# Performance work log

Hardware: AMD Instinct MI355X
Metric: run time of the kernel (lower is better)

## Reference

```python
import jax, jax.numpy as jnp
import numpy as np

INIT_RANGE = 0.02

def setup_inputs() -> dict:
    key = jax.random.key(0)
    ks = jax.random.split(key, 5)
    B, S, D, H, Dh = 4, 2048, 768, 12, 64
    residual = jax.random.normal(ks[0], (B, S, D), dtype=jnp.float32)
    W_Q = jax.random.normal(ks[1], (H, D, Dh), dtype=jnp.float32) * INIT_RANGE
    W_K = jax.random.normal(ks[2], (H, D, Dh), dtype=jnp.float32) * INIT_RANGE
    W_V = jax.random.normal(ks[3], (H, D, Dh), dtype=jnp.float32) * INIT_RANGE
    W_O = jax.random.normal(ks[4], (H, Dh, D), dtype=jnp.float32) * INIT_RANGE
    b_Q = jnp.zeros((H, Dh), dtype=jnp.float32)
    b_K = jnp.zeros((H, Dh), dtype=jnp.float32)
    b_V = jnp.zeros((H, Dh), dtype=jnp.float32)
    b_O = jnp.zeros((D,), dtype=jnp.float32)
    return {"residual": residual, "W_Q": W_Q, "W_K": W_K, "W_V": W_V,
            "W_O": W_O, "b_Q": b_Q, "b_K": b_K, "b_V": b_V, "b_O": b_O}

def reference(residual, W_Q, W_K, W_V, W_O, b_Q, b_K, b_V, b_O):
    # residual: [b, s, d]; W_{Q,K,V}: [h, d, dh]; W_O: [h, dh, d]
    d_head = W_Q.shape[-1]
    q = jnp.einsum('bsd,hde->bshe', residual, W_Q) + b_Q  # [b, s, h, dh]
    k = jnp.einsum('bsd,hde->bshe', residual, W_K) + b_K
    v = jnp.einsum('bsd,hde->bshe', residual, W_V) + b_V
    scores = jnp.einsum('bqhe,bkhe->bhqk', q, k) / jnp.sqrt(jnp.float32(d_head))
    S = residual.shape[1]
    causal = jnp.tril(jnp.ones((S, S), dtype=bool))  # True where attending allowed
    scores = jnp.where(causal, scores, -jnp.inf)
    pattern = jax.nn.softmax(scores, axis=-1)  # [b, h, q, k]
    z = jnp.einsum('bkhe,bhqk->bqhe', v, pattern)  # [b, q, h, dh]
    attn_out = jnp.einsum('bqhe,hed->bqd', z, W_O) + b_O
    return attn_out
```

## Files before the change

### kernel.cpp

```cpp
#include <hip/hip_runtime.h>

typedef short short8 __attribute__((ext_vector_type(8)));
typedef float floatx4 __attribute__((ext_vector_type(4)));
typedef unsigned short ushort_t;


__device__ inline ushort_t f2bf(float f) {
  union { float f; unsigned u; } x; x.f = f;
  unsigned u = x.u;
  unsigned r = u + 0x7fffu + ((u >> 16) & 1u);
  return (ushort_t)(r >> 16);
}

__device__ inline unsigned cvtpk(float a, float b) {
  unsigned r;
  asm("v_cvt_pk_bf16_f32 %0, %1, %2" : "=v"(r) : "v"(a), "v"(b));
  return r;
}

__device__ inline float fexp2(float x) {
#if __has_builtin(__builtin_amdgcn_exp2f)
  return __builtin_amdgcn_exp2f(x);
#else
  return exp2f(x);
#endif
}

__device__ inline void async16(const void* g, void* l) {
  __builtin_amdgcn_global_load_lds((const __attribute__((address_space(1))) void*)g,
                                   (__attribute__((address_space(3))) void*)l,
                                   16, 0, 0);
}


__global__ __launch_bounds__(256) void conv_prep(
    const float* __restrict__ x, ushort_t* __restrict__ rx,
    const float* __restrict__ wq, const float* __restrict__ wk, const float* __restrict__ wv,
    const float* __restrict__ wo,
    const float* __restrict__ bq, const float* __restrict__ bk, const float* __restrict__ bv,
    ushort_t* __restrict__ wqkvT, ushort_t* __restrict__ woT, float* __restrict__ bqkv)
{
  __shared__ ushort_t t[64 * 72];
  const int tid = threadIdx.x;
  const int bid0 = blockIdx.x;
  if (bid0 < 6144) {
    int i = bid0 * 256 + tid;
    float4 f = ((const float4*)x)[i];
    ushort4 o;
    o.x = f2bf(f.x); o.y = f2bf(f.y); o.z = f2bf(f.z); o.w = f2bf(f.w);
    ((ushort4*)rx)[i] = o;
    return;
  }
  const int bid = bid0 - 6144;
  if (bid < 432) {
    int m = bid / 144, rem = bid % 144;
    int h = rem / 12, dt = rem % 12;
    int d0 = dt * 64;
    const float* w = (m == 0) ? wq : ((m == 1) ? wk : wv);
    const float* src = w + ((size_t)h * 768 + d0) * 64;
#pragma unroll
    for (int i = 0; i < 4; ++i) {
      int task = i * 256 + tid;
      int row = task >> 4, c4 = task & 15;
      float4 f = *(const float4*)(src + row * 64 + c4 * 4);
      ushort4 o4;
      o4.x = f2bf(f.x); o4.y = f2bf(f.y); o4.z = f2bf(f.z); o4.w = f2bf(f.w);
      *(ushort4*)&t[row * 72 + c4 * 4] = o4;
    }
    __syncthreads();
    ushort_t* dst = wqkvT + ((size_t)m * 768 + h * 64) * 768 + d0;
#pragma unroll
    for (int i = 0; i < 2; ++i) {
      int task = i * 256 + tid;
      int e = task >> 3, sc = task & 7;
      short8 d8;
#pragma unroll
      for (int j = 0; j < 8; ++j) d8[j] = (short)t[(sc * 8 + j) * 72 + e];
      *(short8*)(dst + (size_t)e * 768 + sc * 8) = d8;
    }
  } else if (bid < 576) {
    int b2 = bid - 432;
    int het = b2 / 12, dt = b2 % 12;
    int he0 = het * 64, d0 = dt * 64;
    const float* src = wo + (size_t)he0 * 768 + d0;
#pragma unroll
    for (int i = 0; i < 4; ++i) {
      int task = i * 256 + tid;
      int row = task >> 4, c4 = task & 15;
      float4 f = *(const float4*)(src + (size_t)row * 768 + c4 * 4);
      ushort4 o4;
      o4.x = f2bf(f.x); o4.y = f2bf(f.y); o4.z = f2bf(f.z); o4.w = f2bf(f.w);
      *(ushort4*)&t[row * 72 + c4 * 4] = o4;
    }
    __syncthreads();
    ushort_t* dst = woT + (size_t)d0 * 768 + he0;
#pragma unroll
    for (int i = 0; i < 2; ++i) {
      int task = i * 256 + tid;
      int dd = task >> 3, sc = task & 7;
      short8 d8;
#pragma unroll
      for (int j = 0; j < 8; ++j) d8[j] = (short)t[(sc * 8 + j) * 72 + dd];
      *(short8*)(dst + (size_t)dd * 768 + sc * 8) = d8;
    }
  } else {
    for (int idx = tid; idx < 2304; idx += 256) {
      int m = idx / 768, rem = idx - m * 768;
      const float* bp = (m == 0) ? bq : ((m == 1) ? bk : bv);
      bqkv[idx] = bp[rem];
    }
  }
}


__global__ __launch_bounds__(256) void gemm_qkv(
    const ushort_t* __restrict__ A, const ushort_t* __restrict__ Bt,
    const float* __restrict__ bias,
    ushort_t* __restrict__ q, ushort_t* __restrict__ k, ushort_t* __restrict__ vt)
{
  __shared__ __align__(16) ushort_t sh[32768];
  const int tid = threadIdx.x;
  const int wave = tid >> 6, lane = tid & 63;
  const int ln15 = lane & 15, quad = lane >> 4;
  const int id = blockIdx.x;
  const int xk = id & 7, j = id >> 3;
  const int bx = (xk >> 1) * 16 + (j & 15);
  const int by = (xk & 1) * 9 + (j >> 4);
  const int row0 = bx * 128, col0 = by * 128;
  const int wm = (wave >> 1) * 64, wn = (wave & 1) * 64;

  const int sr = tid >> 3;
  const int sc = (tid & 7) ^ (sr & 7);
  const ushort_t* gA0 = A + (size_t)(row0 + sr) * 768 + sc * 8;
  const ushort_t* gB0 = Bt + (size_t)(col0 + sr) * 768 + sc * 8;

  const int l7 = ln15 & 7;
  const int baA = (wm + ln15) * 64;
  const int baB = (wn + ln15) * 64;
  const int sl0 = (quad ^ l7) * 8;
  const int sl1 = ((quad + 4) ^ l7) * 8;

  floatx4 acc[4][4];
#pragma unroll
  for (int mi = 0; mi < 4; ++mi)
#pragma unroll
    for (int ni = 0; ni < 4; ++ni)
      acc[mi][ni] = (floatx4){0.f, 0.f, 0.f, 0.f};

#pragma unroll
  for (int i = 0; i < 4; ++i) {
    async16(gA0 + i * 32 * 768, &sh[(i * 256 + tid) * 8]);
    async16(gB0 + i * 32 * 768, &sh[16384 + (i * 256 + tid) * 8]);
  }
  __syncthreads();

  for (int kt = 0; kt < 12; ++kt) {
    const int buf = kt & 1;
    if (kt + 1 < 12) {
      ushort_t* dA = &sh[(buf ^ 1) * 8192];
      ushort_t* dB = &sh[16384 + (buf ^ 1) * 8192];
      const ushort_t* ga = gA0 + (kt + 1) * 64;
      const ushort_t* gb = gB0 + (kt + 1) * 64;
#pragma unroll
      for (int i = 0; i < 4; ++i) {
        async16(ga + i * 32 * 768, dA + (i * 256 + tid) * 8);
        async16(gb + i * 32 * 768, dB + (i * 256 + tid) * 8);
      }
    }
    const ushort_t* sA = &sh[buf * 8192];
    const ushort_t* sB = &sh[16384 + buf * 8192];
    short8 af[4][2], bfv[4][2];
#pragma unroll
    for (int mi = 0; mi < 4; ++mi) {
      af[mi][0] = *(const short8*)&sA[baA + mi * 1024 + sl0];
      af[mi][1] = *(const short8*)&sA[baA + mi * 1024 + sl1];
    }
#pragma unroll
    for (int ni = 0; ni < 4; ++ni) {
      bfv[ni][0] = *(const short8*)&sB[baB + ni * 1024 + sl0];
      bfv[ni][1] = *(const short8*)&sB[baB + ni * 1024 + sl1];
    }
#pragma unroll
    for (int mi = 0; mi < 4; ++mi)
#pragma unroll
      for (int ni = 0; ni < 4; ++ni) {
        acc[mi][ni] = __builtin_amdgcn_mfma_f32_16x16x32_bf16(af[mi][0], bfv[ni][0], acc[mi][ni], 0, 0, 0);
        acc[mi][ni] = __builtin_amdgcn_mfma_f32_16x16x32_bf16(af[mi][1], bfv[ni][1], acc[mi][ni], 0, 0, 0);
      }
    __syncthreads();
  }

  if (col0 < 1536) {
    const float qscale = 0.125f * 1.44269504f;
#pragma unroll
    for (int mi = 0; mi < 4; ++mi) {
#pragma unroll
      for (int ni = 0; ni < 4; ++ni) {
        int gr = row0 + wm + mi * 16 + quad * 4;
        int gc = col0 + wn + ni * 16 + ln15;
        float bia = bias[gc];
        int m = gc / 768;
        int rem = gc - m * 768;
        int h = rem >> 6, e = rem & 63;
        ushort_t* dp = (m == 0) ? q : k;
#pragma unroll
        for (int r = 0; r < 4; ++r) {
          float val = acc[mi][ni][r] + bia;
          int rr = gr + r;
          int bb = rr >> 11, ss = rr & 2047;
          size_t dst = ((size_t)((bb * 12 + h) * 2048 + ss) << 6) + e;
          dp[dst] = f2bf((m == 0) ? val * qscale : val);
        }
      }
    }
  } else {
#pragma unroll
    for (int mi = 0; mi < 4; ++mi) {
#pragma unroll
      for (int ni = 0; ni < 4; ++ni) {
        int col = wn + ni * 16 + ln15;
        int rowb = wm + mi * 16 + quad * 4;
        int rowc = rowb >> 2;
        int msw = (col & 7) << 2;
        float bia = bias[col0 + col];
        ushort4 w4;
        w4.x = f2bf(acc[mi][ni][0] + bia);
        w4.y = f2bf(acc[mi][ni][1] + bia);
        w4.z = f2bf(acc[mi][ni][2] + bia);
        w4.w = f2bf(acc[mi][ni][3] + bia);
        *(ushort4*)&sh[col * 128 + ((rowc ^ msw) << 2)] = w4;
      }
    }
    __syncthreads();
    const int relc0 = col0 - 1536;
    const int bb = row0 >> 11, s0 = row0 & 2047;
#pragma unroll
    for (int i = 0; i < 8; ++i) {
      int g = i * 256 + tid;
      int col = g >> 4, chunk = g & 15;
      int msw = (col & 7) << 2;
      short8 d = *(const short8*)&sh[col * 128 + (((chunk * 2) ^ msw) << 2)];
      int hh = (relc0 + col) >> 6;
      int ee = col & 63;
      *(short8*)(vt + (((size_t)(bb * 12 + hh) * 64 + ee) << 11) + s0 + chunk * 8) = d;
    }
  }
}


__global__ __launch_bounds__(256) void gemm_out(
    const ushort_t* __restrict__ A, const ushort_t* __restrict__ Bt,
    const float* __restrict__ bias, float* __restrict__ outf)
{
  __shared__ __align__(16) ushort_t sh[24576];
  const int tid = threadIdx.x;
  const int wave = tid >> 6, lane = tid & 63;
  const int ln15 = lane & 15, quad = lane >> 4;
  const int id = blockIdx.x;
  const int xk = id & 7, j = id >> 3;
  const int bx = xk * 16 + (j & 15);
  const int by = j >> 4;
  const int row0 = bx * 64, col0 = by * 128;
  const int wm = (wave >> 1) * 32, wn = (wave & 1) * 64;

  const int sr = tid >> 3;
  const int sc = (tid & 7) ^ (sr & 7);
  const ushort_t* gA0 = A + (size_t)(row0 + sr) * 768 + sc * 8;
  const ushort_t* gB0 = Bt + (size_t)(col0 + sr) * 768 + sc * 8;

  const int l7 = ln15 & 7;
  const int baA = (wm + ln15) * 64;
  const int baB = (wn + ln15) * 64;
  const int sl0 = (quad ^ l7) * 8;
  const int sl1 = ((quad + 4) ^ l7) * 8;

  floatx4 acc[2][4];
#pragma unroll
  for (int mi = 0; mi < 2; ++mi)
#pragma unroll
    for (int ni = 0; ni < 4; ++ni)
      acc[mi][ni] = (floatx4){0.f, 0.f, 0.f, 0.f};

#pragma unroll
  for (int i = 0; i < 2; ++i)
    async16(gA0 + i * 32 * 768, &sh[(i * 256 + tid) * 8]);
#pragma unroll
  for (int i = 0; i < 4; ++i)
    async16(gB0 + i * 32 * 768, &sh[8192 + (i * 256 + tid) * 8]);
  __syncthreads();

  for (int kt = 0; kt < 12; ++kt) {
    const int buf = kt & 1;
    if (kt + 1 < 12) {
      ushort_t* dA = &sh[(buf ^ 1) * 4096];
      ushort_t* dB = &sh[8192 + (buf ^ 1) * 8192];
      const ushort_t* ga = gA0 + (kt + 1) * 64;
      const ushort_t* gb = gB0 + (kt + 1) * 64;
#pragma unroll
      for (int i = 0; i < 2; ++i)
        async16(ga + i * 32 * 768, dA + (i * 256 + tid) * 8);
#pragma unroll
      for (int i = 0; i < 4; ++i)
        async16(gb + i * 32 * 768, dB + (i * 256 + tid) * 8);
    }
    const ushort_t* sA = &sh[buf * 4096];
    const ushort_t* sB = &sh[8192 + buf * 8192];
    short8 af[2][2], bfv[4][2];
#pragma unroll
    for (int mi = 0; mi < 2; ++mi) {
      af[mi][0] = *(const short8*)&sA[baA + mi * 1024 + sl0];
      af[mi][1] = *(const short8*)&sA[baA + mi * 1024 + sl1];
    }
#pragma unroll
    for (int ni = 0; ni < 4; ++ni) {
      bfv[ni][0] = *(const short8*)&sB[baB + ni * 1024 + sl0];
      bfv[ni][1] = *(const short8*)&sB[baB + ni * 1024 + sl1];
    }
#pragma unroll
    for (int mi = 0; mi < 2; ++mi)
#pragma unroll
      for (int ni = 0; ni < 4; ++ni) {
        acc[mi][ni] = __builtin_amdgcn_mfma_f32_16x16x32_bf16(af[mi][0], bfv[ni][0], acc[mi][ni], 0, 0, 0);
        acc[mi][ni] = __builtin_amdgcn_mfma_f32_16x16x32_bf16(af[mi][1], bfv[ni][1], acc[mi][ni], 0, 0, 0);
      }
    __syncthreads();
  }

#pragma unroll
  for (int mi = 0; mi < 2; ++mi) {
#pragma unroll
    for (int ni = 0; ni < 4; ++ni) {
      int gr = row0 + wm + mi * 16 + quad * 4;
      int gc = col0 + wn + ni * 16 + ln15;
      float bia = bias[gc];
#pragma unroll
      for (int r = 0; r < 4; ++r)
        outf[(size_t)(gr + r) * 768 + gc] = acc[mi][ni][r] + bia;
    }
  }
}


__device__ inline short8 frag_ld(const ushort_t* t, int row, int ch) {
  return *(const short8*)&t[row * 64 + (((ch ^ row) & 7) * 8)];
}

__global__ __launch_bounds__(256) void attn3(
    const ushort_t* __restrict__ Q, const ushort_t* __restrict__ K,
    const ushort_t* __restrict__ VT, ushort_t* __restrict__ Z)
{
  __shared__ ushort_t lK[2][64 * 64];
  __shared__ ushort_t lV[2][64 * 64];
  const int tid = threadIdx.x;
  const int wave = tid >> 6, lane = tid & 63;
  const int ln15 = lane & 15, quad = lane >> 4;
  const int bi = blockIdx.x;
  const int bh = bi % 48;
  const int t = 15 - (bi / 48);
  const int h = bh % 12, b = bh / 12;
  const size_t base = (size_t)bh * 2048 * 64;
  const ushort_t* Qp = Q + base + (size_t)t * 128 * 64;
  const ushort_t* Kp = K + base;
  const ushort_t* Vp = VT + base;
  const int nk = 2 * t + 2;

  const int srow = tid >> 3, slch = tid & 7;
  const int sc_ = slch ^ (srow & 7);
  const int krow = (srow & 3) | ((srow & 0x0C) << 1) | ((srow & 0x10) >> 2);

#pragma unroll
  for (int i = 0; i < 4; ++i) {
    int task = i * 256 + tid;
    int row = task >> 3;
    int c = slch ^ (row & 7);
    ushort_t* qdst = (row < 64) ? &lK[1][row * 64 + slch * 8]
                                : &lV[1][(row - 64) * 64 + slch * 8];
    async16(Qp + row * 64 + c * 8, qdst);
  }
  async16(Kp + (size_t)krow * 64 + sc_ * 8, &lK[0][tid * 8]);
  async16(Kp + (size_t)(krow + 32) * 64 + sc_ * 8, &lK[0][(256 + tid) * 8]);
  async16(Vp + (size_t)srow * 2048 + sc_ * 8, &lV[0][tid * 8]);
  async16(Vp + (size_t)(srow + 32) * 2048 + sc_ * 8, &lV[0][(256 + tid) * 8]);

  const ushort_t* kPre0 = Kp + (size_t)(64 + krow) * 64 + sc_ * 8;
  const ushort_t* kPre1 = kPre0 + 32 * 64;
  const ushort_t* vPre0 = Vp + (size_t)srow * 2048 + 64 + sc_ * 8;
  const ushort_t* vPre1 = vPre0 + 32 * 2048;

  __syncthreads();
  const ushort_t* qbase = (wave < 2) ? &lK[1][0] : &lV[1][0];
  const int qrl = (wave & 1) * 32;
  short8 qf[2][2];
#pragma unroll
  for (int c = 0; c < 2; ++c) {
    qf[c][0] = frag_ld(qbase, qrl + c * 16 + ln15, quad);
    qf[c][1] = frag_ld(qbase, qrl + c * 16 + ln15, quad + 4);
  }
  __syncthreads();

  float l_i[2] = {0.f, 0.f};
  floatx4 o[2][4];
#pragma unroll
  for (int c = 0; c < 2; ++c)
#pragma unroll
    for (int et = 0; et < 4; ++et) o[c][et] = (floatx4){0.f, 0.f, 0.f, 0.f};

  const int qg0 = t * 128 + wave * 32 + ln15;

  for (int kt = 0; kt < nk; ++kt) {
    const int buf = kt & 1;
    if (kt + 1 < nk) {
      ushort_t* dK = lK[buf ^ 1];
      ushort_t* dV = lV[buf ^ 1];
      async16(kPre0, dK + tid * 8);
      async16(kPre1, dK + (256 + tid) * 8);
      async16(vPre0, dV + tid * 8);
      async16(vPre1, dV + (256 + tid) * 8);
      kPre0 += 4096; kPre1 += 4096; vPre0 += 64; vPre1 += 64;
    }

    floatx4 st[2][4];
#pragma unroll
    for (int ni = 0; ni < 4; ++ni) {
      short8 kf0 = frag_ld(lK[buf], ni * 16 + ln15, quad);
      short8 kf1 = frag_ld(lK[buf], ni * 16 + ln15, quad + 4);
#pragma unroll
      for (int c = 0; c < 2; ++c) {
        floatx4 z4 = (floatx4){0.f, 0.f, 0.f, 0.f};
        z4 = __builtin_amdgcn_mfma_f32_16x16x32_bf16(kf0, qf[c][0], z4, 0, 0, 0);
        st[c][ni] = __builtin_amdgcn_mfma_f32_16x16x32_bf16(kf1, qf[c][1], z4, 0, 0, 0);
      }
    }

    const bool masked = (kt >= 2 * t);
    short8 pf[2][2];
#pragma unroll
    for (int c = 0; c < 2; ++c) {
      const int qg = qg0 + c * 16;
      float p[16];
      float rs = 0.f;
#pragma unroll
      for (int ni = 0; ni < 4; ++ni) {
#pragma unroll
        for (int r = 0; r < 4; ++r) {
          float x = st[c][ni][r];
          if (masked) {
            int kg = kt * 64 + (ni >> 1) * 32 + quad * 8 + (ni & 1) * 4 + r;
            x = (kg <= qg) ? x : -1e30f;
          }
          p[ni * 4 + r] = fexp2(x);
        }
        rs += (p[ni * 4 + 0] + p[ni * 4 + 1]) + (p[ni * 4 + 2] + p[ni * 4 + 3]);
      }
      rs += __shfl_xor(rs, 16);
      rs += __shfl_xor(rs, 32);
      l_i[c] += rs;
      union { unsigned u[4]; short8 s8; } w0, w1;
#pragma unroll
      for (int i2 = 0; i2 < 4; ++i2) {
        w0.u[i2] = cvtpk(p[i2 * 2], p[i2 * 2 + 1]);
        w1.u[i2] = cvtpk(p[8 + i2 * 2], p[8 + i2 * 2 + 1]);
      }
      pf[c][0] = w0.s8;
      pf[c][1] = w1.s8;
    }

#pragma unroll
    for (int et = 0; et < 4; ++et) {
      short8 vf0 = frag_ld(lV[buf], et * 16 + ln15, quad);
      short8 vf1 = frag_ld(lV[buf], et * 16 + ln15, quad + 4);
#pragma unroll
      for (int c = 0; c < 2; ++c) {
        o[c][et] = __builtin_amdgcn_mfma_f32_16x16x32_bf16(vf0, pf[c][0], o[c][et], 0, 0, 0);
        o[c][et] = __builtin_amdgcn_mfma_f32_16x16x32_bf16(vf1, pf[c][1], o[c][et], 0, 0, 0);
      }
    }
    __syncthreads();
  }

#pragma unroll
  for (int c = 0; c < 2; ++c) {
    float inv = 1.f / l_i[c];
    size_t zrow = (size_t)(b * 2048 + t * 128 + wave * 32 + c * 16 + ln15);
#pragma unroll
    for (int et = 0; et < 4; ++et) {
      ushort4 w;
      w.x = f2bf(o[c][et][0] * inv);
      w.y = f2bf(o[c][et][1] * inv);
      w.z = f2bf(o[c][et][2] * inv);
      w.w = f2bf(o[c][et][3] * inv);
      *(ushort4*)&Z[zrow * 768 + h * 64 + et * 16 + quad * 4] = w;
    }
  }
}


extern "C" void kernel_launch(void* const* d_in, const int* in_sizes, int n_in,
                              void* d_out, int out_size, void* d_ws, size_t ws_size,
                              hipStream_t stream)
{
  const float* residual = (const float*)d_in[0];
  const float* W_Q = (const float*)d_in[1];
  const float* W_K = (const float*)d_in[2];
  const float* W_V = (const float*)d_in[3];
  const float* W_O = (const float*)d_in[4];
  const float* b_Q = (const float*)d_in[5];
  const float* b_K = (const float*)d_in[6];
  const float* b_V = (const float*)d_in[7];
  const float* b_O = (const float*)d_in[8];
  float* out = (float*)d_out;

  char* w = (char*)d_ws;
  ushort_t* rx    = (ushort_t*)(w + 0);
  ushort_t* wqkvT = (ushort_t*)(w + 12582912);
  ushort_t* woT   = (ushort_t*)(w + 16121856);
  float*    bqkv  = (float*)   (w + 17301504);
  ushort_t* q     = (ushort_t*)(w + 17310720);
  ushort_t* k     = (ushort_t*)(w + 29893632);
  ushort_t* vt    = (ushort_t*)(w + 55059456);
  ushort_t* z     = rx;

  conv_prep<<<6721, 256, 0, stream>>>(residual, rx, W_Q, W_K, W_V, W_O,
                                      b_Q, b_K, b_V, wqkvT, woT, bqkv);
  gemm_qkv<<<1152, 256, 0, stream>>>(rx, wqkvT, bqkv, q, k, vt);
  attn3<<<768, 256, 0, stream>>>(q, k, vt, z);
  gemm_out<<<768, 256, 0, stream>>>(z, woT, b_O, out);
}
```

Measured before the change: 192.3 us.

## Drop LDS staging in attention; use one-wave blocks loading K/V fragments directly

The attention kernel switches from 256-thread blocks that stage K/V tiles through double-buffered shared memory to 64-thread single-wave blocks. Each block handles a 32-row query group and loads Q, K and V MFMA fragments straight from global memory into registers. This removes LDS traffic and block-wide barriers and gives finer-grained causal load balancing with 3072 blocks. The cost is that K/V tiles are no longer shared across waves, so global/L2 traffic rises roughly fourfold. Loads are also no longer prefetched asynchronously, which exposes memory latency.

After: 245.8 us. +27.8%, slower.

```diff
diff --git a/kernel.cpp b/kernel.cpp
--- a/kernel.cpp
+++ b/kernel.cpp
@@ -341,62 +341,38 @@
 }
 
 
-__device__ inline short8 frag_ld(const ushort_t* t, int row, int ch) {
-  return *(const short8*)&t[row * 64 + (((ch ^ row) & 7) * 8)];
-}
-
-__global__ __launch_bounds__(256) void attn3(
+__global__ __launch_bounds__(64) void attn3(
     const ushort_t* __restrict__ Q, const ushort_t* __restrict__ K,
     const ushort_t* __restrict__ VT, ushort_t* __restrict__ Z)
 {
-  __shared__ ushort_t lK[2][64 * 64];
-  __shared__ ushort_t lV[2][64 * 64];
-  const int tid = threadIdx.x;
-  const int wave = tid >> 6, lane = tid & 63;
+  const int lane = threadIdx.x & 63;
   const int ln15 = lane & 15, quad = lane >> 4;
   const int bi = blockIdx.x;
   const int bh = bi % 48;
-  const int t = 15 - (bi / 48);
+  const int g = 63 - bi / 48;
   const int h = bh % 12, b = bh / 12;
   const size_t base = (size_t)bh * 2048 * 64;
-  const ushort_t* Qp = Q + base + (size_t)t * 128 * 64;
+  const ushort_t* Qp = Q + base + (size_t)g * 32 * 64;
   const ushort_t* Kp = K + base;
   const ushort_t* Vp = VT + base;
-  const int nk = 2 * t + 2;
-
-  const int srow = tid >> 3, slch = tid & 7;
-  const int sc_ = slch ^ (srow & 7);
-  const int krow = (srow & 3) | ((srow & 0x0C) << 1) | ((srow & 0x10) >> 2);
-
-#pragma unroll
-  for (int i = 0; i < 4; ++i) {
-    int task = i * 256 + tid;
-    int row = task >> 3;
-    int c = slch ^ (row & 7);
-    ushort_t* qdst = (row < 64) ? &lK[1][row * 64 + slch * 8]
-                                : &lV[1][(row - 64) * 64 + slch * 8];
-    async16(Qp + row * 64 + c * 8, qdst);
-  }
-  async16(Kp + (size_t)krow * 64 + sc_ * 8, &lK[0][tid * 8]);
-  async16(Kp + (size_t)(krow + 32) * 64 + sc_ * 8, &lK[0][(256 + tid) * 8]);
-  async16(Vp + (size_t)srow * 2048 + sc_ * 8, &lV[0][tid * 8]);
-  async16(Vp + (size_t)(srow + 32) * 2048 + sc_ * 8, &lV[0][(256 + tid) * 8]);
-
-  const ushort_t* kPre0 = Kp + (size_t)(64 + krow) * 64 + sc_ * 8;
-  const ushort_t* kPre1 = kPre0 + 32 * 64;
-  const ushort_t* vPre0 = Vp + (size_t)srow * 2048 + 64 + sc_ * 8;
-  const ushort_t* vPre1 = vPre0 + 32 * 2048;
-
-  __syncthreads();
-  const ushort_t* qbase = (wave < 2) ? &lK[1][0] : &lV[1][0];
-  const int qrl = (wave & 1) * 32;
+  const int nk = (g >> 1) + 1;
+
+  int kap[4];
+#pragma unroll
+  for (int ni = 0; ni < 4; ++ni)
+    kap[ni] = ((ln15 & 3) | ((ln15 & 12) << 1) | ((ni & 1) << 2) | ((ni >> 1) << 5)) * 64;
+
+  int vof[4];
+#pragma unroll
+  for (int et = 0; et < 4; ++et)
+    vof[et] = (et * 16 + ln15) * 2048 + quad * 8;
+
   short8 qf[2][2];
 #pragma unroll
   for (int c = 0; c < 2; ++c) {
-    qf[c][0] = frag_ld(qbase, qrl + c * 16 + ln15, quad);
-    qf[c][1] = frag_ld(qbase, qrl + c * 16 + ln15, quad + 4);
-  }
-  __syncthreads();
+    qf[c][0] = *(const short8*)(Qp + (c * 16 + ln15) * 64 + quad * 8);
+    qf[c][1] = *(const short8*)(Qp + (c * 16 + ln15) * 64 + quad * 8 + 32);
+  }
 
   float l_i[2] = {0.f, 0.f};
   floatx4 o[2][4];
@@ -405,34 +381,36 @@
 #pragma unroll
     for (int et = 0; et < 4; ++et) o[c][et] = (floatx4){0.f, 0.f, 0.f, 0.f};
 
-  const int qg0 = t * 128 + wave * 32 + ln15;
+  const int qg0 = g * 32 + ln15;
 
   for (int kt = 0; kt < nk; ++kt) {
-    const int buf = kt & 1;
-    if (kt + 1 < nk) {
-      ushort_t* dK = lK[buf ^ 1];
-      ushort_t* dV = lV[buf ^ 1];
-      async16(kPre0, dK + tid * 8);
-      async16(kPre1, dK + (256 + tid) * 8);
-      async16(vPre0, dV + tid * 8);
-      async16(vPre1, dV + (256 + tid) * 8);
-      kPre0 += 4096; kPre1 += 4096; vPre0 += 64; vPre1 += 64;
+    const ushort_t* kp = Kp + kt * 4096;
+    const ushort_t* vp = Vp + kt * 64;
+
+    short8 kf[4][2], vf[4][2];
+#pragma unroll
+    for (int ni = 0; ni < 4; ++ni) {
+      kf[ni][0] = *(const short8*)(kp + kap[ni] + quad * 8);
+      kf[ni][1] = *(const short8*)(kp + kap[ni] + quad * 8 + 32);
+    }
+#pragma unroll
+    for (int et = 0; et < 4; ++et) {
+      vf[et][0] = *(const short8*)(vp + vof[et]);
+      vf[et][1] = *(const short8*)(vp + vof[et] + 32);
     }
 
     floatx4 st[2][4];
 #pragma unroll
     for (int ni = 0; ni < 4; ++ni) {
-      short8 kf0 = frag_ld(lK[buf], ni * 16 + ln15, quad);
-      short8 kf1 = frag_ld(lK[buf], ni * 16 + ln15, quad + 4);
 #pragma unroll
       for (int c = 0; c < 2; ++c) {
         floatx4 z4 = (floatx4){0.f, 0.f, 0.f, 0.f};
-        z4 = __builtin_amdgcn_mfma_f32_16x16x32_bf16(kf0, qf[c][0], z4, 0, 0, 0);
-        st[c][ni] = __builtin_amdgcn_mfma_f32_16x16x32_bf16(kf1, qf[c][1], z4, 0, 0, 0);
-      }
-    }
-
-    const bool masked = (kt >= 2 * t);
+        z4 = __builtin_amdgcn_mfma_f32_16x16x32_bf16(kf[ni][0], qf[c][0], z4, 0, 0, 0);
+        st[c][ni] = __builtin_amdgcn_mfma_f32_16x16x32_bf16(kf[ni][1], qf[c][1], z4, 0, 0, 0);
+      }
+    }
+
+    const bool masked = (kt == nk - 1);
     short8 pf[2][2];
 #pragma unroll
     for (int c = 0; c < 2; ++c) {
@@ -467,21 +445,18 @@
 
 #pragma unroll
     for (int et = 0; et < 4; ++et) {
-      short8 vf0 = frag_ld(lV[buf], et * 16 + ln15, quad);
-      short8 vf1 = frag_ld(lV[buf], et * 16 + ln15, quad + 4);
 #pragma unroll
       for (int c = 0; c < 2; ++c) {
-        o[c][et] = __builtin_amdgcn_mfma_f32_16x16x32_bf16(vf0, pf[c][0], o[c][et], 0, 0, 0);
-        o[c][et] = __builtin_amdgcn_mfma_f32_16x16x32_bf16(vf1, pf[c][1], o[c][et], 0, 0, 0);
-      }
-    }
-    __syncthreads();
+        o[c][et] = __builtin_amdgcn_mfma_f32_16x16x32_bf16(vf[et][0], pf[c][0], o[c][et], 0, 0, 0);
+        o[c][et] = __builtin_amdgcn_mfma_f32_16x16x32_bf16(vf[et][1], pf[c][1], o[c][et], 0, 0, 0);
+      }
+    }
   }
 
 #pragma unroll
   for (int c = 0; c < 2; ++c) {
     float inv = 1.f / l_i[c];
-    size_t zrow = (size_t)(b * 2048 + t * 128 + wave * 32 + c * 16 + ln15);
+    size_t zrow = (size_t)(b * 2048 + g * 32 + c * 16 + ln15);
 #pragma unroll
     for (int et = 0; et < 4; ++et) {
       ushort4 w;
@@ -523,6 +498,6 @@
   conv_prep<<<6721, 256, 0, stream>>>(residual, rx, W_Q, W_K, W_V, W_O,
                                       b_Q, b_K, b_V, wqkvT, woT, bqkv);
   gemm_qkv<<<1152, 256, 0, stream>>>(rx, wqkvT, bqkv, q, k, vt);
-  attn3<<<768, 256, 0, stream>>>(q, k, vt, z);
+  attn3<<<3072, 64, 0, stream>>>(q, k, vt, z);
   gemm_out<<<768, 256, 0, stream>>>(z, woT, b_O, out);
 }
```
